# Optimization experiments

Hardware: AMD Instinct MI355X
Metric: run time of the kernel (lower is better)

## Reference

```python
import jax, jax.numpy as jnp
import numpy as np

N = 100000     # graph nodes (users + items)
NNZ = 3200000  # edges, avg degree 32
D = 128        # latent_dim
H = 64         # latent_dim // 2


def setup_inputs() -> dict:
    key = jax.random.key(0)
    ks = jax.random.split(key, 6)
    x = jax.random.normal(ks[0], (N, D), jnp.float32)
    rows = jax.random.randint(ks[1], (NNZ,), 0, N, jnp.int32)
    cols = jax.random.randint(ks[2], (NNZ,), 0, N, jnp.int32)
    # positive values ~ normalized adjacency weights
    vals = jax.random.uniform(ks[3], (NNZ,), jnp.float32) / 32.0
    # torch Linear convention: weight [out, in], xavier-uniform init, bias 0.01
    W1 = jax.random.normal(ks[4], (H, D), jnp.float32) * (6.0 / (D + H)) ** 0.5
    b1 = jnp.full((H,), 0.01, jnp.float32)
    W2 = jax.random.normal(ks[5], (1, H), jnp.float32) * (6.0 / (H + 1)) ** 0.5
    b2 = jnp.full((1,), 0.01, jnp.float32)
    t = jnp.zeros((1,), jnp.float32)  # ODE time, unused by the math
    return dict(t=t, x=x, rows=rows, cols=cols, vals=vals, W1=W1, b1=b1, W2=W2, b2=b2)


def _spmm(rows, cols, vals, x):
    # sparse (COO) @ dense: out[r] += vals[e] * x[cols[e]] for edges e with rows[e]==r
    return jax.ops.segment_sum(vals[:, None] * x[cols], rows, num_segments=x.shape[0])


def reference(t, x, rows, cols, vals, W1, b1, W2, b2):
    # gate: sigmoid(Linear(clamp(Linear(x))))  -> [N, 1]
    hidden = jnp.clip(x @ W1.T + b1, -10.0, 10.0)
    alph = jax.nn.sigmoid(hidden @ W2.T + b2)
    alph = jnp.clip(alph, 1e-6, 1.0 - 1e-6)
    # two-hop graph diffusion: alph * (A @ (A @ x)) - x
    ax = _spmm(rows, cols, vals, x)
    ax = alph * _spmm(rows, cols, vals, ax)
    return ax - x
```

## Files before the change

### kernel.cpp

```cpp
#include <hip/hip_runtime.h>
#include <stdint.h>

typedef unsigned int uint;
typedef unsigned short ushort;
typedef float f32x2 __attribute__((ext_vector_type(2)));
typedef float f32x4v __attribute__((ext_vector_type(4)));
typedef short short8 __attribute__((ext_vector_type(8)));

#define NBC_MAX 512
#define NBLK 1024
#define VAL7_SCALE 4064.0f
#define VAL7_INV   (1.0f / 4064.0f)

__device__ __forceinline__ ushort f2bf(float f) {
    uint u = __float_as_uint(f);
    return (ushort)((u + 0x7fffu + ((u >> 16) & 1u)) >> 16);
}


__global__ __launch_bounds__(512) void k_count(const int* __restrict__ rows,
                                               uint* __restrict__ C, int nnz, int nb) {
    __shared__ uint lh[NBC_MAX];
    long long beg = ((long long)blockIdx.x * nnz) / gridDim.x;
    long long end = ((long long)(blockIdx.x + 1) * nnz) / gridDim.x;
    for (int j = threadIdx.x; j < nb; j += blockDim.x) lh[j] = 0;
    __syncthreads();
    {
        long long i = beg + threadIdx.x;
        for (; i + 1536 < end; i += 2048) {
            int r0 = __builtin_nontemporal_load(rows + i);
            int r1 = __builtin_nontemporal_load(rows + i + 512);
            int r2 = __builtin_nontemporal_load(rows + i + 1024);
            int r3 = __builtin_nontemporal_load(rows + i + 1536);
            atomicAdd(&lh[r0 >> 8], 1u);
            atomicAdd(&lh[r1 >> 8], 1u);
            atomicAdd(&lh[r2 >> 8], 1u);
            atomicAdd(&lh[r3 >> 8], 1u);
        }
        for (; i < end; i += 512)
            atomicAdd(&lh[__builtin_nontemporal_load(rows + i) >> 8], 1u);
    }
    __syncthreads();
    for (int j = threadIdx.x; j < nb; j += blockDim.x)
        C[(size_t)blockIdx.x * nb + j] = lh[j];
}


__global__ __launch_bounds__(256) void k_cscan(uint* __restrict__ C,
                                               uint* __restrict__ T, int nb) {
    int wv = (blockIdx.x * blockDim.x + threadIdx.x) >> 6;
    int lane = threadIdx.x & 63;
    if (wv >= nb) return;
    uint v[16];
    uint s = 0;
#pragma unroll
    for (int k = 0; k < 16; k++) {
        v[k] = C[(size_t)(lane * 16 + k) * nb + wv];
        s += v[k];
    }
    uint inc = s;
#pragma unroll
    for (int o = 1; o < 64; o <<= 1) { uint u = __shfl_up(inc, o); if (lane >= o) inc += u; }
    uint run = inc - s;
#pragma unroll
    for (int k = 0; k < 16; k++) {
        uint t = v[k];
        C[(size_t)(lane * 16 + k) * nb + wv] = run;
        run += t;
    }
    if (lane == 63) T[wv] = inc;
}


__global__ __launch_bounds__(256) void k_scan(const uint* __restrict__ T,
                                              uint* __restrict__ off,
                                              uint* __restrict__ row_off,
                                              int nb, int nnz, int N) {
    __shared__ uint wsum[4];
    __shared__ uint carry;
    int t = threadIdx.x, lane = t & 63, wv = t >> 6;
    if (t == 0) carry = 0;
    __syncthreads();
    for (int base = 0; base < nb; base += 256) {
        int i = base + t;
        uint v = (i < nb) ? T[i] : 0u;
        uint inc = v;
#pragma unroll
        for (int o = 1; o < 64; o <<= 1) { uint u = __shfl_up(inc, o); if (lane >= o) inc += u; }
        if (lane == 63) wsum[wv] = inc;
        __syncthreads();
        uint woff = 0;
        for (int k = 0; k < wv; k++) woff += wsum[k];
        uint excl = carry + woff + (inc - v);
        if (i < nb) off[i] = excl;
        uint tot = wsum[0] + wsum[1] + wsum[2] + wsum[3];
        __syncthreads();
        if (t == 0) carry += tot;
        __syncthreads();
    }
    if (t == 0) { off[nb] = (uint)nnz; row_off[N] = (uint)nnz; }
}


__global__ __launch_bounds__(512) void k_scatter(const int* __restrict__ rows,
                                                 const int* __restrict__ cols,
                                                 const float* __restrict__ vals,
                                                 const uint* __restrict__ C,
                                                 const uint* __restrict__ boff,
                                                 uint* __restrict__ stage,
                                                 int nnz, int nb) {
    __shared__ uint lh[NBC_MAX];
    __shared__ uint gb[NBC_MAX];
    long long beg = ((long long)blockIdx.x * nnz) / gridDim.x;
    long long end = ((long long)(blockIdx.x + 1) * nnz) / gridDim.x;
    for (int j = threadIdx.x; j < nb; j += blockDim.x) {
        lh[j] = 0;
        gb[j] = boff[j] + C[(size_t)blockIdx.x * nb + j];
    }
    __syncthreads();
    {
        long long i = beg + threadIdx.x;
        for (; i + 1536 < end; i += 2048) {
            int r0 = __builtin_nontemporal_load(rows + i);
            int r1 = __builtin_nontemporal_load(rows + i + 512);
            int r2 = __builtin_nontemporal_load(rows + i + 1024);
            int r3 = __builtin_nontemporal_load(rows + i + 1536);
            uint c0 = (uint)__builtin_nontemporal_load(cols + i);
            uint c1 = (uint)__builtin_nontemporal_load(cols + i + 512);
            uint c2 = (uint)__builtin_nontemporal_load(cols + i + 1024);
            uint c3 = (uint)__builtin_nontemporal_load(cols + i + 1536);
            float v0 = __builtin_nontemporal_load(vals + i);
            float v1 = __builtin_nontemporal_load(vals + i + 512);
            float v2 = __builtin_nontemporal_load(vals + i + 1024);
            float v3 = __builtin_nontemporal_load(vals + i + 1536);
            uint p0 = gb[r0 >> 8] + atomicAdd(&lh[r0 >> 8], 1u);
            uint p1 = gb[r1 >> 8] + atomicAdd(&lh[r1 >> 8], 1u);
            uint p2 = gb[r2 >> 8] + atomicAdd(&lh[r2 >> 8], 1u);
            uint p3 = gb[r3 >> 8] + atomicAdd(&lh[r3 >> 8], 1u);
            uint q0 = (uint)fminf(v0 * VAL7_SCALE + 0.5f, 127.f);
            uint q1 = (uint)fminf(v1 * VAL7_SCALE + 0.5f, 127.f);
            uint q2 = (uint)fminf(v2 * VAL7_SCALE + 0.5f, 127.f);
            uint q3 = (uint)fminf(v3 * VAL7_SCALE + 0.5f, 127.f);
            stage[p0] = ((uint)(r0 & 255) << 24) | (c0 << 7) | q0;
            stage[p1] = ((uint)(r1 & 255) << 24) | (c1 << 7) | q1;
            stage[p2] = ((uint)(r2 & 255) << 24) | (c2 << 7) | q2;
            stage[p3] = ((uint)(r3 & 255) << 24) | (c3 << 7) | q3;
        }
        for (; i < end; i += 512) {
            int r = __builtin_nontemporal_load(rows + i);
            int b = r >> 8;
            uint pos = gb[b] + atomicAdd(&lh[b], 1u);
            uint c = (uint)__builtin_nontemporal_load(cols + i);
            float v = __builtin_nontemporal_load(vals + i);
            uint q = (uint)fminf(v * VAL7_SCALE + 0.5f, 127.f);
            stage[pos] = ((uint)(r & 255) << 24) | (c << 7) | q;
        }
    }
}


__global__ __launch_bounds__(1024) void k_bsort(const uint* __restrict__ boff,
                                                const uint* __restrict__ stage,
                                                uint* __restrict__ sorted,
                                                uint* __restrict__ row_off,
                                                int N) {
    __shared__ uint rcnt[256], rcur[256];
    __shared__ uint wsum[4];
    int b = blockIdx.x;
    uint s = boff[b], e = boff[b + 1];
    int t = threadIdx.x;
    if (t < 256) rcnt[t] = 0;
    __syncthreads();
    for (uint i = s + t; i < e; i += blockDim.x)
        atomicAdd(&rcnt[stage[i] >> 24], 1u);
    __syncthreads();
    int lane = t & 63, wv = t >> 6;
    uint v = 0, inc = 0;
    if (t < 256) {
        v = rcnt[t];
        inc = v;
#pragma unroll
        for (int o = 1; o < 64; o <<= 1) { uint u = __shfl_up(inc, o); if (lane >= o) inc += u; }
        if (lane == 63) wsum[wv] = inc;
    }
    __syncthreads();
    if (t < 256) {
        uint woff = 0;
        for (int k = 0; k < wv; k++) woff += wsum[k];
        uint excl = woff + inc - v;
        rcur[t] = excl;
        int r = (b << 8) + t;
        if (r < N) row_off[r] = s + excl;
    }
    __syncthreads();
    for (uint i = s + t; i < e; i += blockDim.x) {
        uint rec = stage[i];
        uint pos = atomicAdd(&rcur[rec >> 24], 1u);
        sorted[s + pos] = rec & 0x00FFFFFFu;
    }
}


__global__ __launch_bounds__(256) void k_gatemfma(const float* __restrict__ x,
                                                  const float* __restrict__ W1,
                                                  const float* __restrict__ b1,
                                                  const float* __restrict__ W2,
                                                  const float* __restrict__ b2,
                                                  float* __restrict__ alph,
                                                  unsigned char* __restrict__ xf8, int N) {
    int lane = threadIdx.x & 63;
    int gw = (blockIdx.x * blockDim.x + threadIdx.x) >> 6;
    int nwaves = (gridDim.x * blockDim.x) >> 6;
    int g = lane >> 4;
    int r16 = lane & 15;

    short8 Bfrag[4][4];
#pragma unroll
    for (int c = 0; c < 4; c++) {
        const float* wrow = W1 + (size_t)(c * 16 + r16) * 128 + g * 8;
#pragma unroll
        for (int t = 0; t < 4; t++) {
            float4 f0 = *(const float4*)(wrow + t * 32);
            float4 f1 = *(const float4*)(wrow + t * 32 + 4);
            short8 s;
            s[0] = (short)f2bf(f0.x); s[1] = (short)f2bf(f0.y);
            s[2] = (short)f2bf(f0.z); s[3] = (short)f2bf(f0.w);
            s[4] = (short)f2bf(f1.x); s[5] = (short)f2bf(f1.y);
            s[6] = (short)f2bf(f1.z); s[7] = (short)f2bf(f1.w);
            Bfrag[c][t] = s;
        }
    }
    float b1c[4], w2c[4];
#pragma unroll
    for (int c = 0; c < 4; c++) { b1c[c] = b1[c * 16 + r16]; w2c[c] = W2[c * 16 + r16]; }
    float b2s = b2[0];

    int ntiles = (N + 15) >> 4;
    for (int tile = gw; tile < ntiles; tile += nwaves) {
        int n0 = tile << 4;
        int nrow = n0 + r16;
        int nclamp = nrow < N ? nrow : N - 1;
        const float* xrow = x + ((size_t)nclamp << 7) + g * 8;
        f32x4v acc0 = {0.f, 0.f, 0.f, 0.f}, acc1 = {0.f, 0.f, 0.f, 0.f};
        f32x4v acc2 = {0.f, 0.f, 0.f, 0.f}, acc3 = {0.f, 0.f, 0.f, 0.f};
#pragma unroll
        for (int t = 0; t < 4; t++) {
            float4 f0 = *(const float4*)(xrow + t * 32);
            float4 f1 = *(const float4*)(xrow + t * 32 + 4);
            if (nrow < N) {
                int pk0 = __builtin_amdgcn_cvt_pk_fp8_f32(f0.x, f0.y, 0, false);
                pk0 = __builtin_amdgcn_cvt_pk_fp8_f32(f0.z, f0.w, pk0, true);
                int pk1 = __builtin_amdgcn_cvt_pk_fp8_f32(f1.x, f1.y, 0, false);
                pk1 = __builtin_amdgcn_cvt_pk_fp8_f32(f1.z, f1.w, pk1, true);
                uint* xb = (uint*)(xf8 + ((size_t)nrow << 7) + t * 32 + g * 8);
                xb[0] = (uint)pk0;
                xb[1] = (uint)pk1;
            }
            short8 A;
            A[0] = (short)f2bf(f0.x); A[1] = (short)f2bf(f0.y);
            A[2] = (short)f2bf(f0.z); A[3] = (short)f2bf(f0.w);
            A[4] = (short)f2bf(f1.x); A[5] = (short)f2bf(f1.y);
            A[6] = (short)f2bf(f1.z); A[7] = (short)f2bf(f1.w);
            acc0 = __builtin_amdgcn_mfma_f32_16x16x32_bf16(A, Bfrag[0][t], acc0, 0, 0, 0);
            acc1 = __builtin_amdgcn_mfma_f32_16x16x32_bf16(A, Bfrag[1][t], acc1, 0, 0, 0);
            acc2 = __builtin_amdgcn_mfma_f32_16x16x32_bf16(A, Bfrag[2][t], acc2, 0, 0, 0);
            acc3 = __builtin_amdgcn_mfma_f32_16x16x32_bf16(A, Bfrag[3][t], acc3, 0, 0, 0);
        }
        float pr0 = 0.f, pr1 = 0.f, pr2 = 0.f, pr3 = 0.f;
#pragma unroll
        for (int r = 0; r < 4; r++) {
            float h0 = fminf(fmaxf(acc0[r] + b1c[0], -10.f), 10.f) * w2c[0];
            float h1 = fminf(fmaxf(acc1[r] + b1c[1], -10.f), 10.f) * w2c[1];
            float h2 = fminf(fmaxf(acc2[r] + b1c[2], -10.f), 10.f) * w2c[2];
            float h3 = fminf(fmaxf(acc3[r] + b1c[3], -10.f), 10.f) * w2c[3];
            float s = (h0 + h1) + (h2 + h3);
            if (r == 0) pr0 = s; else if (r == 1) pr1 = s;
            else if (r == 2) pr2 = s; else pr3 = s;
        }
#pragma unroll
        for (int o = 1; o < 16; o <<= 1) {
            pr0 += __shfl_xor(pr0, o);
            pr1 += __shfl_xor(pr1, o);
            pr2 += __shfl_xor(pr2, o);
            pr3 += __shfl_xor(pr3, o);
        }
        if (r16 < 4) {
            float p = r16 == 0 ? pr0 : r16 == 1 ? pr1 : r16 == 2 ? pr2 : pr3;
            float a = 1.f / (1.f + __expf(-(p + b2s)));
            a = fminf(fmaxf(a, 1e-6f), 1.f - 1e-6f);
            int node = n0 + g * 4 + r16;
            if (node < N) alph[node] = a;
        }
    }
}


__global__ __launch_bounds__(256) void k_spmm1(const uint* __restrict__ roff,
                                               const uint* __restrict__ recs,
                                               const unsigned char* __restrict__ xf8,
                                               unsigned char* __restrict__ axf8, int N) {
    int w = (blockIdx.x * blockDim.x + threadIdx.x) >> 6;
    int lane = threadIdx.x & 63;
    if (w >= N) return;
    uint beg = (uint)__builtin_amdgcn_readfirstlane(roff[w]);
    uint end = (uint)__builtin_amdgcn_readfirstlane(roff[w + 1]);
    float s0[8], s1[8];
#pragma unroll
    for (int k = 0; k < 8; k++) { s0[k] = 0.f; s1[k] = 0.f; }
    uint e = beg;
    for (; e + 8 <= end; e += 8) {
#pragma unroll
        for (int k = 0; k < 8; k++) {
            uint q = __builtin_nontemporal_load(recs + e + k);
            ushort u = *(const ushort*)(xf8 + ((size_t)(q >> 7) << 7) + (lane << 1));
            float v = (float)(q & 0x7Fu) * VAL7_INV;
            f32x2 f = __builtin_amdgcn_cvt_pk_f32_fp8((int)u, false);
            s0[k] = fmaf(v, f.x, s0[k]);
            s1[k] = fmaf(v, f.y, s1[k]);
        }
    }
    for (; e < end; e++) {
        uint q = __builtin_nontemporal_load(recs + e);
        ushort u = *(const ushort*)(xf8 + ((size_t)(q >> 7) << 7) + (lane << 1));
        float v = (float)(q & 0x7Fu) * VAL7_INV;
        f32x2 f = __builtin_amdgcn_cvt_pk_f32_fp8((int)u, false);
        s0[0] = fmaf(v, f.x, s0[0]);
        s1[0] = fmaf(v, f.y, s1[0]);
    }
    float a0 = ((s0[0] + s0[1]) + (s0[2] + s0[3])) + ((s0[4] + s0[5]) + (s0[6] + s0[7]));
    float a1 = ((s1[0] + s1[1]) + (s1[2] + s1[3])) + ((s1[4] + s1[5]) + (s1[6] + s1[7]));
    int pk = __builtin_amdgcn_cvt_pk_fp8_f32(a0, a1, 0, false);
    *(ushort*)(axf8 + ((size_t)w << 7) + (lane << 1)) = (ushort)(pk & 0xffff);
}


__global__ __launch_bounds__(256) void k_spmm2(const uint* __restrict__ roff,
                                               const uint* __restrict__ recs,
                                               const unsigned char* __restrict__ axf8,
                                               const float* __restrict__ alph,
                                               const float* __restrict__ x,
                                               float* __restrict__ out, int N) {
    int w = (blockIdx.x * blockDim.x + threadIdx.x) >> 6;
    int lane = threadIdx.x & 63;
    if (w >= N) return;
    uint beg = (uint)__builtin_amdgcn_readfirstlane(roff[w]);
    uint end = (uint)__builtin_amdgcn_readfirstlane(roff[w + 1]);
    float s0[8], s1[8];
#pragma unroll
    for (int k = 0; k < 8; k++) { s0[k] = 0.f; s1[k] = 0.f; }
    uint e = beg;
    for (; e + 8 <= end; e += 8) {
#pragma unroll
        for (int k = 0; k < 8; k++) {
            uint q = __builtin_nontemporal_load(recs + e + k);
            ushort u = *(const ushort*)(axf8 + ((size_t)(q >> 7) << 7) + (lane << 1));
            float v = (float)(q & 0x7Fu) * VAL7_INV;
            f32x2 f = __builtin_amdgcn_cvt_pk_f32_fp8((int)u, false);
            s0[k] = fmaf(v, f.x, s0[k]);
            s1[k] = fmaf(v, f.y, s1[k]);
        }
    }
    for (; e < end; e++) {
        uint q = __builtin_nontemporal_load(recs + e);
        ushort u = *(const ushort*)(axf8 + ((size_t)(q >> 7) << 7) + (lane << 1));
        float v = (float)(q & 0x7Fu) * VAL7_INV;
        f32x2 f = __builtin_amdgcn_cvt_pk_f32_fp8((int)u, false);
        s0[0] = fmaf(v, f.x, s0[0]);
        s1[0] = fmaf(v, f.y, s1[0]);
    }
    float a0 = ((s0[0] + s0[1]) + (s0[2] + s0[3])) + ((s0[4] + s0[5]) + (s0[6] + s0[7]));
    float a1 = ((s1[0] + s1[1]) + (s1[2] + s1[3])) + ((s1[4] + s1[5]) + (s1[6] + s1[7]));
    float al = alph[w];
    const f32x2* xp = (const f32x2*)(x + ((size_t)w << 7)) + lane;
    f32x2 xr = __builtin_nontemporal_load(xp);
    f32x2 o;
    o.x = fmaf(al, a0, -xr.x);
    o.y = fmaf(al, a1, -xr.y);
    __builtin_nontemporal_store(o, (f32x2*)out + ((size_t)w << 6) + lane);
}


extern "C" void kernel_launch(void* const* d_in, const int* in_sizes, int n_in,
                              void* d_out, int out_size, void* d_ws, size_t ws_size,
                              hipStream_t stream) {
    const float* x    = (const float*)d_in[1];
    const int*   rows = (const int*)d_in[2];
    const int*   cols = (const int*)d_in[3];
    const float* vals = (const float*)d_in[4];
    const float* W1 = (const float*)d_in[5];
    const float* b1 = (const float*)d_in[6];
    const float* W2 = (const float*)d_in[7];
    const float* b2 = (const float*)d_in[8];
    float* out = (float*)d_out;

    int N = in_sizes[1] / 128;
    int nnz = in_sizes[2];
    int nb = (N + 255) >> 8;

    char* ws = (char*)d_ws;
    size_t off_b = 0;
    auto take = [&](size_t bytes) -> char* {
        size_t p = (off_b + 255) & ~(size_t)255;
        off_b = p + bytes;
        return ws + p;
    };
    uint*   stage  = (uint*)take((size_t)nnz * 4);
    unsigned char* xf8 = (unsigned char*)take((size_t)N * 128);
    uint*   sorted = (uint*)take((size_t)nnz * 4);
    unsigned char* axf8 = (unsigned char*)take((size_t)N * 128);
    float*  alph   = (float*)take((size_t)N * 4);
    uint*   C      = (uint*)take((size_t)NBLK * nb * 4);
    uint*   T      = (uint*)take((size_t)(nb + 1) * 4);
    uint*   boff   = (uint*)take((size_t)(nb + 1) * 4);
    uint*   row_off = (uint*)take((size_t)(N + 1) * 4);
    (void)ws_size; (void)n_in; (void)out_size;

    int cscan_blocks = (nb * 64 + 255) / 256;

    k_count<<<NBLK, 512, 0, stream>>>(rows, C, nnz, nb);
    k_cscan<<<cscan_blocks, 256, 0, stream>>>(C, T, nb);
    k_scan<<<1, 256, 0, stream>>>(T, boff, row_off, nb, nnz, N);
    k_scatter<<<NBLK, 512, 0, stream>>>(rows, cols, vals, C, boff, stage, nnz, nb);
    k_bsort<<<nb, 1024, 0, stream>>>(boff, stage, sorted, row_off, N);
    k_gatemfma<<<512, 256, 0, stream>>>(x, W1, b1, W2, b2, alph, xf8, N);
    k_spmm1<<<((N * 64) + 255) / 256, 256, 0, stream>>>(row_off, sorted, xf8, axf8, N);
    k_spmm2<<<((N * 64) + 255) / 256, 256, 0, stream>>>(row_off, sorted, axf8, alph, x, out, N);
}
```

Measured before the change: 251.7 us.

## Process two edges per wave with 4-byte gathers and per-wave bucket-sort counters

The SpMM kernels now split each 64-lane wave into two halves, each half handling a different edge and gathering 4 fp8 features per lane, with a cross-half shuffle reduction at the end. The aim is wider gather loads and more edges in flight per wave. The bucket sort kernel gets per-wave private histograms and scatter counters to cut LDS atomic contention, at the price of larger shared memory and a 16-way prefix per row. Occupancy hints are also added to the SpMM kernels.

```diff
diff --git a/kernel.cpp b/kernel.cpp
--- a/kernel.cpp
+++ b/kernel.cpp
@@ -164,39 +164,52 @@
                                                 uint* __restrict__ sorted,
                                                 uint* __restrict__ row_off,
                                                 int N) {
-    __shared__ uint rcnt[256], rcur[256];
+    __shared__ uint rcnt[16][256];
     __shared__ uint wsum[4];
     int b = blockIdx.x;
     uint s = boff[b], e = boff[b + 1];
     int t = threadIdx.x;
-    if (t < 256) rcnt[t] = 0;
-    __syncthreads();
-    for (uint i = s + t; i < e; i += blockDim.x)
-        atomicAdd(&rcnt[stage[i] >> 24], 1u);
-    __syncthreads();
-    int lane = t & 63, wv = t >> 6;
+    int wv16 = t >> 6;
+    for (int k = t; k < 16 * 256; k += 1024) ((uint*)rcnt)[k] = 0;
+    __syncthreads();
+    for (uint i = s + t; i < e; i += 1024)
+        atomicAdd(&rcnt[wv16][stage[i] >> 24], 1u);
+    __syncthreads();
+    uint cex[16];
+    uint rtot = 0;
+    if (t < 256) {
+#pragma unroll
+        for (int k = 0; k < 16; k++) {
+            uint c = rcnt[k][t];
+            cex[k] = rtot;
+            rtot += c;
+        }
+    }
+    __syncthreads();
+    int lane = t & 63, wv4 = t >> 6;
     uint v = 0, inc = 0;
     if (t < 256) {
-        v = rcnt[t];
+        v = rtot;
         inc = v;
 #pragma unroll
         for (int o = 1; o < 64; o <<= 1) { uint u = __shfl_up(inc, o); if (lane >= o) inc += u; }
-        if (lane == 63) wsum[wv] = inc;
+        if (lane == 63) wsum[wv4] = inc;
     }
     __syncthreads();
     if (t < 256) {
         uint woff = 0;
-        for (int k = 0; k < wv; k++) woff += wsum[k];
+        for (int k = 0; k < wv4; k++) woff += wsum[k];
         uint excl = woff + inc - v;
-        rcur[t] = excl;
         int r = (b << 8) + t;
         if (r < N) row_off[r] = s + excl;
-    }
-    __syncthreads();
-    for (uint i = s + t; i < e; i += blockDim.x) {
+#pragma unroll
+        for (int k = 0; k < 16; k++) rcnt[k][t] = s + excl + cex[k];
+    }
+    __syncthreads();
+    for (uint i = s + t; i < e; i += 1024) {
         uint rec = stage[i];
-        uint pos = atomicAdd(&rcur[rec >> 24], 1u);
-        sorted[s + pos] = rec & 0x00FFFFFFu;
+        uint pos = atomicAdd(&rcnt[wv16][rec >> 24], 1u);
+        sorted[pos] = rec & 0x00FFFFFFu;
     }
 }
 
@@ -295,88 +308,108 @@
 }
 
 
-__global__ __launch_bounds__(256) void k_spmm1(const uint* __restrict__ roff,
-                                               const uint* __restrict__ recs,
-                                               const unsigned char* __restrict__ xf8,
-                                               unsigned char* __restrict__ axf8, int N) {
+__global__ __launch_bounds__(256, 8) void k_spmm1(const uint* __restrict__ roff,
+                                                  const uint* __restrict__ recs,
+                                                  const unsigned char* __restrict__ xf8,
+                                                  unsigned char* __restrict__ axf8, int N) {
     int w = (blockIdx.x * blockDim.x + threadIdx.x) >> 6;
     int lane = threadIdx.x & 63;
     if (w >= N) return;
+    int half = lane >> 5, l5 = lane & 31;
     uint beg = (uint)__builtin_amdgcn_readfirstlane(roff[w]);
     uint end = (uint)__builtin_amdgcn_readfirstlane(roff[w + 1]);
-    float s0[8], s1[8];
-#pragma unroll
-    for (int k = 0; k < 8; k++) { s0[k] = 0.f; s1[k] = 0.f; }
+    f32x4v A0 = {0.f, 0.f, 0.f, 0.f}, A1 = {0.f, 0.f, 0.f, 0.f};
+    f32x4v A2 = {0.f, 0.f, 0.f, 0.f}, A3 = {0.f, 0.f, 0.f, 0.f};
+    auto pair = [&](uint e, f32x4v& A) {
+        uint q0 = __builtin_nontemporal_load(recs + e);
+        uint q1 = __builtin_nontemporal_load(recs + e + 1);
+        uint qs = half ? q1 : q0;
+        float vs = (float)(qs & 0x7Fu) * VAL7_INV;
+        uint g = *(const uint*)(xf8 + ((size_t)(qs >> 7) << 7) + (l5 << 2));
+        f32x2 fa = __builtin_amdgcn_cvt_pk_f32_fp8((int)g, false);
+        f32x2 fb = __builtin_amdgcn_cvt_pk_f32_fp8((int)g, true);
+        A.x = fmaf(vs, fa.x, A.x); A.y = fmaf(vs, fa.y, A.y);
+        A.z = fmaf(vs, fb.x, A.z); A.w = fmaf(vs, fb.y, A.w);
+    };
     uint e = beg;
     for (; e + 8 <= end; e += 8) {
-#pragma unroll
-        for (int k = 0; k < 8; k++) {
-            uint q = __builtin_nontemporal_load(recs + e + k);
-            ushort u = *(const ushort*)(xf8 + ((size_t)(q >> 7) << 7) + (lane << 1));
-            float v = (float)(q & 0x7Fu) * VAL7_INV;
-            f32x2 f = __builtin_amdgcn_cvt_pk_f32_fp8((int)u, false);
-            s0[k] = fmaf(v, f.x, s0[k]);
-            s1[k] = fmaf(v, f.y, s1[k]);
-        }
-    }
-    for (; e < end; e++) {
-        uint q = __builtin_nontemporal_load(recs + e);
-        ushort u = *(const ushort*)(xf8 + ((size_t)(q >> 7) << 7) + (lane << 1));
-        float v = (float)(q & 0x7Fu) * VAL7_INV;
-        f32x2 f = __builtin_amdgcn_cvt_pk_f32_fp8((int)u, false);
-        s0[0] = fmaf(v, f.x, s0[0]);
-        s1[0] = fmaf(v, f.y, s1[0]);
-    }
-    float a0 = ((s0[0] + s0[1]) + (s0[2] + s0[3])) + ((s0[4] + s0[5]) + (s0[6] + s0[7]));
-    float a1 = ((s1[0] + s1[1]) + (s1[2] + s1[3])) + ((s1[4] + s1[5]) + (s1[6] + s1[7]));
-    int pk = __builtin_amdgcn_cvt_pk_fp8_f32(a0, a1, 0, false);
-    *(ushort*)(axf8 + ((size_t)w << 7) + (lane << 1)) = (ushort)(pk & 0xffff);
-}
-
-
-__global__ __launch_bounds__(256) void k_spmm2(const uint* __restrict__ roff,
-                                               const uint* __restrict__ recs,
-                                               const unsigned char* __restrict__ axf8,
-                                               const float* __restrict__ alph,
-                                               const float* __restrict__ x,
-                                               float* __restrict__ out, int N) {
+        pair(e, A0); pair(e + 2, A1); pair(e + 4, A2); pair(e + 6, A3);
+    }
+    for (; e + 2 <= end; e += 2) pair(e, A0);
+    if (e < end) {
+        uint q0 = __builtin_nontemporal_load(recs + e);
+        float vs = half ? 0.f : (float)(q0 & 0x7Fu) * VAL7_INV;
+        uint g = *(const uint*)(xf8 + ((size_t)(q0 >> 7) << 7) + (l5 << 2));
+        f32x2 fa = __builtin_amdgcn_cvt_pk_f32_fp8((int)g, false);
+        f32x2 fb = __builtin_amdgcn_cvt_pk_f32_fp8((int)g, true);
+        A1.x = fmaf(vs, fa.x, A1.x); A1.y = fmaf(vs, fa.y, A1.y);
+        A1.z = fmaf(vs, fb.x, A1.z); A1.w = fmaf(vs, fb.y, A1.w);
+    }
+    A0 += A1; A2 += A3; A0 += A2;
+    A0.x += __shfl_xor(A0.x, 32);
+    A0.y += __shfl_xor(A0.y, 32);
+    A0.z += __shfl_xor(A0.z, 32);
+    A0.w += __shfl_xor(A0.w, 32);
+    int pk = __builtin_amdgcn_cvt_pk_fp8_f32(A0.x, A0.y, 0, false);
+    pk = __builtin_amdgcn_cvt_pk_fp8_f32(A0.z, A0.w, pk, true);
+    if (half == 0) ((uint*)(axf8 + ((size_t)w << 7)))[l5] = (uint)pk;
+}
+
+
+__global__ __launch_bounds__(256, 8) void k_spmm2(const uint* __restrict__ roff,
+                                                  const uint* __restrict__ recs,
+                                                  const unsigned char* __restrict__ axf8,
+                                                  const float* __restrict__ alph,
+                                                  const float* __restrict__ x,
+                                                  float* __restrict__ out, int N) {
     int w = (blockIdx.x * blockDim.x + threadIdx.x) >> 6;
     int lane = threadIdx.x & 63;
     if (w >= N) return;
+    int half = lane >> 5, l5 = lane & 31;
     uint beg = (uint)__builtin_amdgcn_readfirstlane(roff[w]);
     uint end = (uint)__builtin_amdgcn_readfirstlane(roff[w + 1]);
-    float s0[8], s1[8];
-#pragma unroll
-    for (int k = 0; k < 8; k++) { s0[k] = 0.f; s1[k] = 0.f; }
+    f32x4v A0 = {0.f, 0.f, 0.f, 0.f}, A1 = {0.f, 0.f, 0.f, 0.f};
+    f32x4v A2 = {0.f, 0.f, 0.f, 0.f}, A3 = {0.f, 0.f, 0.f, 0.f};
+    auto pair = [&](uint e, f32x4v& A) {
+        uint q0 = __builtin_nontemporal_load(recs + e);
+        uint q1 = __builtin_nontemporal_load(recs + e + 1);
+        uint qs = half ? q1 : q0;
+        float vs = (float)(qs & 0x7Fu) * VAL7_INV;
+        uint g = *(const uint*)(axf8 + ((size_t)(qs >> 7) << 7) + (l5 << 2));
+        f32x2 fa = __builtin_amdgcn_cvt_pk_f32_fp8((int)g, false);
+        f32x2 fb = __builtin_amdgcn_cvt_pk_f32_fp8((int)g, true);
+        A.x = fmaf(vs, fa.x, A.x); A.y = fmaf(vs, fa.y, A.y);
+        A.z = fmaf(vs, fb.x, A.z); A.w = fmaf(vs, fb.y, A.w);
+    };
     uint e = beg;
     for (; e + 8 <= end; e += 8) {
-#pragma unroll
-        for (int k = 0; k < 8; k++) {
-            uint q = __builtin_nontemporal_load(recs + e + k);
-            ushort u = *(const ushort*)(axf8 + ((size_t)(q >> 7) << 7) + (lane << 1));
-            float v = (float)(q & 0x7Fu) * VAL7_INV;
-            f32x2 f = __builtin_amdgcn_cvt_pk_f32_fp8((int)u, false);
-            s0[k] = fmaf(v, f.x, s0[k]);
-            s1[k] = fmaf(v, f.y, s1[k]);
-        }
-    }
-    for (; e < end; e++) {
-        uint q = __builtin_nontemporal_load(recs + e);
-        ushort u = *(const ushort*)(axf8 + ((size_t)(q >> 7) << 7) + (lane << 1));
-        float v = (float)(q & 0x7Fu) * VAL7_INV;
-        f32x2 f = __builtin_amdgcn_cvt_pk_f32_fp8((int)u, false);
-        s0[0] = fmaf(v, f.x, s0[0]);
-        s1[0] = fmaf(v, f.y, s1[0]);
-    }
-    float a0 = ((s0[0] + s0[1]) + (s0[2] + s0[3])) + ((s0[4] + s0[5]) + (s0[6] + s0[7]));
-    float a1 = ((s1[0] + s1[1]) + (s1[2] + s1[3])) + ((s1[4] + s1[5]) + (s1[6] + s1[7]));
+        pair(e, A0); pair(e + 2, A1); pair(e + 4, A2); pair(e + 6, A3);
+    }
+    for (; e + 2 <= end; e += 2) pair(e, A0);
+    if (e < end) {
+        uint q0 = __builtin_nontemporal_load(recs + e);
+        float vs = half ? 0.f : (float)(q0 & 0x7Fu) * VAL7_INV;
+        uint g = *(const uint*)(axf8 + ((size_t)(q0 >> 7) << 7) + (l5 << 2));
+        f32x2 fa = __builtin_amdgcn_cvt_pk_f32_fp8((int)g, false);
+        f32x2 fb = __builtin_amdgcn_cvt_pk_f32_fp8((int)g, true);
+        A1.x = fmaf(vs, fa.x, A1.x); A1.y = fmaf(vs, fa.y, A1.y);
+        A1.z = fmaf(vs, fb.x, A1.z); A1.w = fmaf(vs, fb.y, A1.w);
+    }
+    A0 += A1; A2 += A3; A0 += A2;
+    A0.x += __shfl_xor(A0.x, 32);
+    A0.y += __shfl_xor(A0.y, 32);
+    A0.z += __shfl_xor(A0.z, 32);
+    A0.w += __shfl_xor(A0.w, 32);
     float al = alph[w];
-    const f32x2* xp = (const f32x2*)(x + ((size_t)w << 7)) + lane;
-    f32x2 xr = __builtin_nontemporal_load(xp);
-    f32x2 o;
-    o.x = fmaf(al, a0, -xr.x);
-    o.y = fmaf(al, a1, -xr.y);
-    __builtin_nontemporal_store(o, (f32x2*)out + ((size_t)w << 6) + lane);
+    const f32x4v* xp = (const f32x4v*)(x + ((size_t)w << 7)) + l5;
+    f32x4v xr = __builtin_nontemporal_load(xp);
+    f32x4v o;
+    o.x = fmaf(al, A0.x, -xr.x);
+    o.y = fmaf(al, A0.y, -xr.y);
+    o.z = fmaf(al, A0.z, -xr.z);
+    o.w = fmaf(al, A0.w, -xr.w);
+    if (half == 0)
+        __builtin_nontemporal_store(o, (f32x4v*)(out + ((size_t)w << 7)) + l5);
 }
 
 
```

New measurement: 239.1 us. 5.0% less time.
